# Optimization experiments

Hardware: AMD Instinct MI355X
Metric: run time of the kernel (lower is better)

The kernel has to match this reference:

```python
import jax, jax.numpy as jnp
import numpy as np

B, T, TM = 4, 1024, 1500
D_MODEL, D_FFN, H, D_HEAD, D_MEM = 1024, 4096, 16, 64, 1024
EPS = 1e-5


def layernorm(x, g):
    m = jnp.mean(x, axis=-1, keepdims=True)
    xc = x - m
    v = jnp.mean(xc * xc, axis=-1, keepdims=True)
    return xc * jax.lax.rsqrt(v + EPS) * g


def setup_inputs() -> dict:
    key = jax.random.key(0)
    ks = jax.random.split(key, 12)
    s = lambda fan_in: 1.0 / np.sqrt(fan_in)
    return {
        "x": jax.random.normal(ks[0], (B, T, D_MODEL), jnp.float32),
        "encoder_output": jax.random.normal(ks[1], (B, TM, D_MEM), jnp.float32),
        "encoder_mask": jax.random.randint(ks[2], (B, TM), 0, 2).astype(bool),
        "w_qkv": jax.random.normal(ks[3], (D_MODEL, 3 * H * D_HEAD), jnp.float32) * s(D_MODEL),
        "w_o_sa": jax.random.normal(ks[4], (H * D_HEAD, D_MODEL), jnp.float32) * s(H * D_HEAD),
        "w_q": jax.random.normal(ks[5], (D_MODEL, H * D_HEAD), jnp.float32) * s(D_MODEL),
        "w_kv": jax.random.normal(ks[6], (D_MEM, 2 * H * D_HEAD), jnp.float32) * s(D_MEM),
        "w_o_xa": jax.random.normal(ks[7], (H * D_HEAD, D_MODEL), jnp.float32) * s(H * D_HEAD),
        "w_ff1": jax.random.normal(ks[8], (D_MODEL, D_FFN), jnp.float32) * s(D_MODEL),
        "w_ff2": jax.random.normal(ks[9], (D_FFN, D_MODEL), jnp.float32) * s(D_FFN),
        "g_sa": jnp.ones((D_MODEL,), jnp.float32),
        "g_xaq": jnp.ones((D_MODEL,), jnp.float32),
        "g_xam": jnp.ones((D_MEM,), jnp.float32),
        "g_ff": jnp.ones((D_MODEL,), jnp.float32),
    }


def reference(x, encoder_output, encoder_mask, w_qkv, w_o_sa, w_q, w_kv, w_o_xa,
              w_ff1, w_ff2, g_sa, g_xaq, g_xam, g_ff):
    b, t, _ = x.shape
    scale = D_HEAD ** -0.5

    # ---- causal self-attention ----
    residual = x
    xn = layernorm(x, g_sa)
    qkv = (xn @ w_qkv).reshape(b, t, 3, H, D_HEAD)
    q, k, v = qkv[:, :, 0], qkv[:, :, 1], qkv[:, :, 2]  # (B,T,H,D)
    scores = jnp.einsum('bqhd,bkhd->bhqk', q, k) * scale
    causal = jnp.tril(jnp.ones((t, t), x.dtype))
    scores = scores + (1.0 - causal) * -1e9
    attn = jax.nn.softmax(scores, axis=-1)
    sa = jnp.einsum('bhqk,bkhd->bqhd', attn, v).reshape(b, t, H * D_HEAD)
    x = residual + sa @ w_o_sa

    # ---- cross-attention ----
    residual = x
    qn = layernorm(x, g_xaq)
    mn = layernorm(encoder_output, g_xam)
    tq, tm = t, mn.shape[1]
    qx = (qn @ w_q).reshape(b, tq, H, D_HEAD)
    kvx = (mn @ w_kv).reshape(b, tm, 2, H, D_HEAD)
    kx, vx = kvx[:, :, 0], kvx[:, :, 1]
    xs = jnp.einsum('bqhd,bkhd->bhqk', qx, kx) * scale
    xs = jnp.where(encoder_mask[:, None, None, :], xs, -jnp.inf)
    xattn = jax.nn.softmax(xs, axis=-1)
    xa = jnp.einsum('bhqk,bkhd->bqhd', xattn, vx).reshape(b, tq, H * D_HEAD)
    x = residual + xa @ w_o_xa

    # ---- pointwise FFN (kernel_size=1 conv == linear) ----
    residual = x
    h = layernorm(x, g_ff)
    h = jax.nn.gelu(h @ w_ff1, approximate=True) @ w_ff2
    x = residual + h
    return (x, k, v)
```

## Files before the change

kernel.cpp:

```cpp
#include <hip/hip_runtime.h>
#include <hip/hip_bf16.h>
#include <cstdint>
#include <cstddef>


typedef __attribute__((ext_vector_type(4))) float f32x4;
typedef __attribute__((ext_vector_type(8))) short s8v;
typedef __attribute__((ext_vector_type(2))) unsigned uint2v;

#define DEVI __device__ __forceinline__

DEVI short f2bf(float f) {
  union { float f; unsigned u; } x; x.f = f;
  unsigned r = x.u + 0x7fffu + ((x.u >> 16) & 1u);
  return (short)(r >> 16);
}
DEVI unsigned cvtpk_bf2(float lo, float hi) {
  unsigned r;
  asm("v_cvt_pk_bf16_f32 %0, %1, %2" : "=v"(r) : "v"(lo), "v"(hi));
  return r;
}
DEVI float fexp2(float x) {
  float r;
  asm("v_exp_f32 %0, %1" : "=v"(r) : "v"(x));
  return r;
}
DEVI float bpermf(int srclane, float v) {
  union { float f; int i; } x; x.f = v;
  x.i = __builtin_amdgcn_ds_bpermute(srclane << 2, x.i);
  return x.f;
}
DEVI void gload_lds16(const void* g, void* l) {
  __builtin_amdgcn_global_load_lds((const __attribute__((address_space(1))) void*)g,
                                   (__attribute__((address_space(3))) void*)l,
                                   16, 0, 0);
}

__global__ __launch_bounds__(256) void k_transpose_cvt(
    const float* __restrict__ w, short* __restrict__ wt, int K, int N) {
  __shared__ float tile[32][33];
  int n0 = blockIdx.x * 32, k0 = blockIdx.y * 32;
  int t = threadIdx.x;
  int row = t >> 3, c4 = (t & 7) * 4;
  *(f32x4*)&tile[row][c4] = *(const f32x4*)(w + (size_t)(k0 + row) * N + n0 + c4);
  __syncthreads();
  float v0 = tile[c4 + 0][row], v1 = tile[c4 + 1][row];
  float v2 = tile[c4 + 2][row], v3 = tile[c4 + 3][row];
  uint2v o = {cvtpk_bf2(v0, v1), cvtpk_bf2(v2, v3)};
  *(uint2v*)(wt + (size_t)(n0 + row) * K + k0 + c4) = o;
}

__global__ __launch_bounds__(256) void k_vtrans(
    const short* __restrict__ src, int srs, int coff,
    short* __restrict__ dst, int T, int Tp) {
  __shared__ short tile[32][72];
  int bh = blockIdx.y, b = bh >> 4, h = bh & 15;
  int t0 = blockIdx.x * 32;
  const short* sB = src + (size_t)b * T * srs + coff + h * 64;
  short* dB = dst + (size_t)bh * 64 * Tp;
  int t = threadIdx.x;
  int r = t >> 3, c = (t & 7) * 8;
  int tr = t0 + r; if (tr > T - 1) tr = T - 1;
  *(s8v*)&tile[r][c] = *(const s8v*)(sB + (size_t)tr * srs + c);
  __syncthreads();
  int d = t & 63, ch = t >> 6;
  s8v o;
#pragma unroll
  for (int j = 0; j < 8; j++) o[j] = tile[ch * 8 + j][d];
  *(s8v*)(dB + (size_t)d * Tp + t0 + ch * 8) = o;
}

__global__ void k_maskpack(const int* __restrict__ mask,
                           unsigned long long* __restrict__ out, int Tk, int mw) {
  int b = blockIdx.x, w = threadIdx.x;
  if (w >= mw) return;
  unsigned long long v = 0;
  const int* mb = mask + (size_t)b * Tk;
#pragma unroll 4
  for (int j = 0; j < 64; j++) {
    int k = w * 64 + j;
    if (k < Tk && mb[k]) v |= (1ull << j);
  }
  out[(size_t)b * mw + w] = v;
}

__global__ __launch_bounds__(256) void k_ln(
    const float* __restrict__ x, const float* __restrict__ g,
    short* __restrict__ out) {
  int row = blockIdx.x;
  const float* xr = x + (size_t)row * 1024;
  int t = threadIdx.x, wid = t >> 6, lane = t & 63;
  f32x4 v = ((const f32x4*)xr)[t];
  float s = v[0] + v[1] + v[2] + v[3];
#pragma unroll
  for (int m = 32; m >= 1; m >>= 1) s += __shfl_xor(s, m);
  __shared__ float red[4];
  if (lane == 0) red[wid] = s;
  __syncthreads();
  float mean = (red[0] + red[1] + red[2] + red[3]) * (1.f / 1024.f);
  float q = 0.f;
#pragma unroll
  for (int i = 0; i < 4; i++) { v[i] -= mean; q += v[i] * v[i]; }
#pragma unroll
  for (int m = 32; m >= 1; m >>= 1) q += __shfl_xor(q, m);
  __syncthreads();
  if (lane == 0) red[wid] = q;
  __syncthreads();
  float var = (red[0] + red[1] + red[2] + red[3]) * (1.f / 1024.f);
  float rs = rsqrtf(var + 1e-5f);
  f32x4 gv = ((const f32x4*)g)[t];
  unsigned w0 = cvtpk_bf2(v[0] * rs * gv[0], v[1] * rs * gv[1]);
  unsigned w1 = cvtpk_bf2(v[2] * rs * gv[2], v[3] * rs * gv[3]);
  uint2v w = {w0, w1};
  *(uint2v*)(out + (size_t)row * 1024 + t * 4) = w;
}

template <bool RES, bool GELU_, bool F32OUT, bool BF16OUT, bool KV>
__global__ __launch_bounds__(256) void k_gemm3(
    const short* __restrict__ A, const short* __restrict__ Bt,
    float* __restrict__ Cf, short* __restrict__ Cb,
    const float* __restrict__ res, float* __restrict__ okv,
    int M, int N, int K, int lda, int ldb) {
  __shared__ short As[128 * 64];
  __shared__ short Bs[128 * 64];
  int z = blockIdx.z;
  A += (size_t)z * K;
  Bt += (size_t)z * K;
  if (F32OUT && !RES) Cf += (size_t)z * (size_t)M * N;

  int bx, by;
  {
    int gx = gridDim.x, gy = gridDim.y;
    int nxy = gx * gy, chunk = nxy >> 3;
    int orig = blockIdx.y * gx + blockIdx.x;
    int gid = (orig & 7) * chunk + (orig >> 3);
    int full = gy << 3, nfull = gx >> 3, lim = nfull * full;
    if (gid < lim) {
      int band = gid / full, r = gid - band * full;
      bx = (band << 3) + (r & 7);
      by = r >> 3;
    } else {
      int r = gid - lim, w = gx - (nfull << 3);
      bx = (nfull << 3) + r % w;
      by = r / w;
    }
  }
  int am = bx * 128, bn = by * 128;

  int t = threadIdx.x, wid = t >> 6, lane = t & 63;
  int la = lane & 15, lb = lane >> 4;
  int wr = wid >> 1, wc = wid & 1;

  const short* gp[8];
  int dof[8];
#pragma unroll
  for (int l = 0; l < 8; l++) {
    int cl = (l & 3) * 256 + t;
    int row = cl >> 3, g = cl & 7;
    int col = (g ^ (row & 7)) << 3;
    if (l < 4) {
      int ar = am + row; if (ar > M - 1) ar = M - 1;
      gp[l] = A + (size_t)ar * lda + col;
    } else {
      gp[l] = Bt + (size_t)(bn + row) * ldb + col;
    }
    dof[l] = ((l & 3) * 256 + wid * 64) * 8;
  }

  int aOff[4], bOff[4];
#pragma unroll
  for (int m = 0; m < 4; m++) {
    int r = wr * 64 + m * 16 + la;
    aOff[m] = r * 64 + ((lb ^ (r & 7)) << 3);
  }
#pragma unroll
  for (int n = 0; n < 4; n++) {
    int r = wc * 64 + n * 16 + la;
    bOff[n] = r * 64 + ((lb ^ (r & 7)) << 3);
  }

  f32x4 acc[4][4];
#pragma unroll
  for (int m = 0; m < 4; m++)
#pragma unroll
    for (int n = 0; n < 4; n++) acc[m][n] = (f32x4){0.f, 0.f, 0.f, 0.f};

  int nk = K >> 6;
  for (int ks = 0; ks < nk; ++ks) {
#pragma unroll
    for (int l = 0; l < 4; l++) { gload_lds16(gp[l], As + dof[l]); gp[l] += 64; }
#pragma unroll
    for (int l = 4; l < 8; l++) { gload_lds16(gp[l], Bs + dof[l]); gp[l] += 64; }
    __syncthreads();
#pragma unroll
    for (int kk = 0; kk < 2; kk++) {
      s8v af[4], bfg[4];
#pragma unroll
      for (int m = 0; m < 4; m++)
        af[m] = *(const s8v*)(As + (aOff[m] ^ (kk << 5)));
#pragma unroll
      for (int n = 0; n < 4; n++)
        bfg[n] = *(const s8v*)(Bs + (bOff[n] ^ (kk << 5)));
#pragma unroll
      for (int m = 0; m < 4; m++)
#pragma unroll
        for (int n = 0; n < 4; n++)
          acc[m][n] = __builtin_amdgcn_mfma_f32_16x16x32_bf16(af[m], bfg[n], acc[m][n], 0, 0, 0);
    }
    __syncthreads();
  }

#pragma unroll
  for (int m = 0; m < 4; m++) {
    int rb = am + wr * 64 + m * 16 + lb * 4;
#pragma unroll
    for (int n = 0; n < 4; n++) {
      int col = bn + wc * 64 + n * 16 + la;
#pragma unroll
      for (int j = 0; j < 4; j++) {
        int r = rb + j;
        if (r < M) {
          float v = acc[m][n][j];
          if (RES) v += res[(size_t)r * N + col];
          if (GELU_) {
            float u = v;
            float y = 0.7978845608f * u * (1.f + 0.044715f * u * u);
            float e = fexp2(fminf(y * 2.88539008f, 80.f));
            float th = (e - 1.f) * __builtin_amdgcn_rcpf(e + 1.f);
            v = 0.5f * u * (1.f + th);
          }
          if (F32OUT) Cf[(size_t)r * N + col] = v;
          if (BF16OUT) Cb[(size_t)r * N + col] = f2bf(v);
          if (KV) {
            if (col >= 2048)
              okv[(size_t)4096 * 1024 + (size_t)r * 1024 + (col - 2048)] = v;
            else if (col >= 1024)
              okv[(size_t)r * 1024 + (col - 1024)] = v;
          }
        }
      }
    }
  }
}

__global__ __launch_bounds__(256) void k_red2b(
    const f32x4* __restrict__ p, short* __restrict__ outb, int n) {
  int i = blockIdx.x * 256 + threadIdx.x;
  f32x4 v = p[i] + p[i + (size_t)n];
  uint2v w = {cvtpk_bf2(v[0], v[1]), cvtpk_bf2(v[2], v[3])};
  *(uint2v*)(outb + (size_t)i * 4) = w;
}

__global__ __launch_bounds__(256) void k_red2ln(
    const f32x4* __restrict__ p, const f32x4* __restrict__ res,
    float* __restrict__ xout, short* __restrict__ nout,
    const float* __restrict__ g, int n) {
  int row = blockIdx.x;
  int t = threadIdx.x, wid = t >> 6, lane = t & 63;
  size_t i = (size_t)row * 256 + t;
  f32x4 v = res[i] + (p[i] + p[i + (size_t)n]);
  ((f32x4*)xout)[i] = v;
  float s = v[0] + v[1] + v[2] + v[3];
#pragma unroll
  for (int m = 32; m >= 1; m >>= 1) s += __shfl_xor(s, m);
  __shared__ float red[4];
  if (lane == 0) red[wid] = s;
  __syncthreads();
  float mean = (red[0] + red[1] + red[2] + red[3]) * (1.f / 1024.f);
  float q = 0.f;
#pragma unroll
  for (int k = 0; k < 4; k++) { v[k] -= mean; q += v[k] * v[k]; }
#pragma unroll
  for (int m = 32; m >= 1; m >>= 1) q += __shfl_xor(q, m);
  __syncthreads();
  if (lane == 0) red[wid] = q;
  __syncthreads();
  float var = (red[0] + red[1] + red[2] + red[3]) * (1.f / 1024.f);
  float rs = rsqrtf(var + 1e-5f);
  f32x4 gv = ((const f32x4*)g)[t];
  uint2v w = {cvtpk_bf2(v[0] * rs * gv[0], v[1] * rs * gv[1]),
              cvtpk_bf2(v[2] * rs * gv[2], v[3] * rs * gv[3])};
  *(uint2v*)(nout + (size_t)row * 1024 + t * 4) = w;
}

template <bool CAUSAL>
__global__ __launch_bounds__(512) void k_attn4(
    const short* __restrict__ qbuf, int qrs,
    const short* __restrict__ kbuf, int krs,
    const short* __restrict__ vT, int vts,
    short* __restrict__ obuf, int ors,
    const unsigned long long* __restrict__ mbits, int mwords,
    int Tq, int Tk, float scale) {
  __shared__ short Ks[64 * 64];
  __shared__ short Vs[64 * 64];
  __shared__ short Ps[8 * 1024];
  int lid = blockIdx.y * gridDim.x + blockIdx.x;
  int rest = lid >> 3;
  int bh = (lid & 7) * 8 + (rest & 7);
  int qsel = rest >> 3;
  int b = bh >> 4, h = bh & 15;
  int t = threadIdx.x, wid = t >> 6, lane = t & 63;
  int la = lane & 15, lb = lane >> 4;
  float lscale = scale * 1.44269504f;

  const short* qB = qbuf + (size_t)b * Tq * qrs + h * 64;
  const short* kB = kbuf + (size_t)b * Tk * krs + h * 64;
  const short* vB = vT + (size_t)bh * 64 * vts;
  char* Pw = (char*)(Ps + wid * 1024);

  int sr = t >> 3, scol = (t & 7) * 8;
  int swz = sr * 64 + (scol ^ ((sr & 7) << 3));

  int nsup = CAUSAL ? 2 : 1;
  for (int s = 0; s < nsup; s++) {
    int st = CAUSAL ? (s ? 7 - qsel : qsel) : qsel;
    int q0 = st * 128 + wid * 16;
    int nkt = CAUSAL ? 2 * st + 2 : (Tk + 63) >> 6;
    int lastkt = CAUSAL ? (q0 >> 6) : nkt - 1;

    s8v qf[2];
#pragma unroll
    for (int kk = 0; kk < 2; kk++)
      qf[kk] = *(const s8v*)(qB + (size_t)(q0 + la) * qrs + kk * 32 + lb * 8);

    f32x4 accO[4];
#pragma unroll
    for (int n = 0; n < 4; n++) accO[n] = (f32x4){0.f, 0.f, 0.f, 0.f};
    float m = -1e30f, l = 0.f;

    s8v krg, vrg;
    {
      int tk = sr; if (tk > Tk - 1) tk = Tk - 1;
      krg = *(const s8v*)(kB + (size_t)tk * krs + scol);
      vrg = *(const s8v*)(vB + (size_t)sr * vts + scol);
    }

    for (int kt = 0; kt < nkt; kt++) {
      int kb0 = kt << 6;
      __syncthreads();
      *(s8v*)&Ks[swz] = krg;
      *(s8v*)&Vs[swz] = vrg;
      __syncthreads();
      if (kt + 1 < nkt) {
        int kb = kb0 + 64;
        int tk = kb + sr; if (tk > Tk - 1) tk = Tk - 1;
        krg = *(const s8v*)(kB + (size_t)tk * krs + scol);
        vrg = *(const s8v*)(vB + (size_t)sr * vts + kb + scol);
      }
      if (kt > lastkt) continue;

      bool needMask;
      unsigned long long wm = ~0ull;
      if (CAUSAL) {
        needMask = (kt == lastkt);
      } else {
        wm = mbits[(size_t)b * mwords + kt];
        needMask = (wm != ~0ull);
      }

      float sc[4][4];
      __builtin_amdgcn_s_setprio(1);
#pragma unroll
      for (int n = 0; n < 4; n++) {
        f32x4 a = (f32x4){0.f, 0.f, 0.f, 0.f};
#pragma unroll
        for (int kk = 0; kk < 2; kk++) {
          s8v kf = *(const s8v*)&Ks[(n * 16 + la) * 64 +
                                    ((kk * 32 + lb * 8) ^ ((la & 7) << 3))];
          a = __builtin_amdgcn_mfma_f32_16x16x32_bf16(kf, qf[kk], a, 0, 0, 0);
        }
#pragma unroll
        for (int j = 0; j < 4; j++) {
          float sv = a[j] * lscale;
          if (needMask) {
            int ki = n * 16 + lb * 4 + j;
            bool ok = CAUSAL ? (kb0 + ki <= q0 + la) : (((wm >> ki) & 1ull) != 0);
            sv = ok ? sv : -1e30f;
          }
          sc[n][j] = sv;
        }
      }
      __builtin_amdgcn_s_setprio(0);

      float tm = sc[0][0];
#pragma unroll
      for (int n = 0; n < 4; n++)
#pragma unroll
        for (int j = 0; j < 4; j++) tm = fmaxf(tm, sc[n][j]);
      tm = fmaxf(tm, __shfl_xor(tm, 16));
      tm = fmaxf(tm, __shfl_xor(tm, 32));
      tm = fmaxf(tm, -1e4f);

      bool skip = __all(tm - m <= 10.f);
      float alpha = 1.f;
      if (!skip) {
        float mn_ = fmaxf(m, tm);
        alpha = fexp2(m - mn_);
        m = mn_;
      }

      unsigned W[4][2];
      float ps = 0.f;
#pragma unroll
      for (int n = 0; n < 4; n++) {
        float p0 = fexp2(sc[n][0] - m), p1 = fexp2(sc[n][1] - m);
        float p2 = fexp2(sc[n][2] - m), p3 = fexp2(sc[n][3] - m);
        ps += (p0 + p1) + (p2 + p3);
        W[n][0] = cvtpk_bf2(p0, p1);
        W[n][1] = cvtpk_bf2(p2, p3);
      }
      ps += __shfl_xor(ps, 16);
      ps += __shfl_xor(ps, 32);
      l = l * alpha + ps;

      if (!skip) {
#pragma unroll
        for (int j = 0; j < 4; j++) {
          float aj = bpermf(lb * 20 + j, alpha);
#pragma unroll
          for (int n = 0; n < 4; n++) accO[n][j] *= aj;
        }
      }

#pragma unroll
      for (int n = 0; n < 4; n++) {
        uint2v w2 = {W[n][0], W[n][1]};
        *(uint2v*)(Pw + ((la * 128 + n * 32 + lb * 8) ^ ((la & 7) << 4))) = w2;
      }
      __builtin_amdgcn_s_setprio(1);
#pragma unroll
      for (int kk = 0; kk < 2; kk++) {
        s8v pa = *(const s8v*)(Pw + ((la * 128 + kk * 64 + lb * 16) ^ ((la & 7) << 4)));
#pragma unroll
        for (int n = 0; n < 4; n++) {
          s8v vf = *(const s8v*)&Vs[(n * 16 + la) * 64 +
                                    ((kk * 32 + lb * 8) ^ ((la & 7) << 3))];
          accO[n] = __builtin_amdgcn_mfma_f32_16x16x32_bf16(pa, vf, accO[n], 0, 0, 0);
        }
      }
      __builtin_amdgcn_s_setprio(0);
    }

#pragma unroll
    for (int j = 0; j < 4; j++) {
      float lj = bpermf(lb * 20 + j, l);
      float inv = 1.f / lj;
      int r = q0 + lb * 4 + j;
#pragma unroll
      for (int n = 0; n < 4; n++)
        obuf[(size_t)(b * Tq + r) * ors + h * 64 + n * 16 + la] = f2bf(accO[n][j] * inv);
    }
  }
}

extern "C" void kernel_launch(void* const* d_in, const int* in_sizes, int n_in,
                              void* d_out, int out_size, void* d_ws, size_t ws_size,
                              hipStream_t stream) {
  (void)in_sizes; (void)n_in; (void)out_size; (void)ws_size;
  const float* x      = (const float*)d_in[0];
  const float* enc    = (const float*)d_in[1];
  const int*   mask   = (const int*)d_in[2];
  const float* w_qkv  = (const float*)d_in[3];
  const float* w_o_sa = (const float*)d_in[4];
  const float* w_q    = (const float*)d_in[5];
  const float* w_kv   = (const float*)d_in[6];
  const float* w_o_xa = (const float*)d_in[7];
  const float* w_ff1  = (const float*)d_in[8];
  const float* w_ff2  = (const float*)d_in[9];
  const float* g_sa   = (const float*)d_in[10];
  const float* g_xaq  = (const float*)d_in[11];
  const float* g_xam  = (const float*)d_in[12];
  const float* g_ff   = (const float*)d_in[13];

  float* out_x = (float*)d_out;
  float* out_k = out_x + (size_t)4096 * 1024;

  char* ws = (char*)d_ws;
  size_t off = 0;
  auto alloc = [&](size_t bytes) -> void* {
    void* p = ws + off;
    off += (bytes + 255) & ~(size_t)255;
    return p;
  };
  short* wqkv_t = (short*)alloc((size_t)3072 * 1024 * 2);
  short* wosa_t = (short*)alloc((size_t)1024 * 1024 * 2);
  short* wq_t   = (short*)alloc((size_t)1024 * 1024 * 2);
  short* wkv_t  = (short*)alloc((size_t)2048 * 1024 * 2);
  short* woxa_t = (short*)alloc((size_t)1024 * 1024 * 2);
  short* wff1_t = (short*)alloc((size_t)4096 * 1024 * 2);
  short* wff2_t = (short*)alloc((size_t)1024 * 4096 * 2);
  short* xn     = (short*)alloc((size_t)4096 * 1024 * 2);
  short* qkv_b  = (short*)alloc((size_t)4096 * 3072 * 2);
  short* sa_b   = (short*)alloc((size_t)4096 * 1024 * 2);
  float* x1     = (float*)alloc((size_t)4096 * 1024 * 4);
  short* qn     = (short*)alloc((size_t)4096 * 1024 * 2);
  short* mn     = (short*)alloc((size_t)6000 * 1024 * 2);
  short* qx_b   = (short*)alloc((size_t)4096 * 1024 * 2);
  short* kvx_b  = (short*)alloc((size_t)6000 * 2048 * 2);
  short* xa_b   = (short*)alloc((size_t)4096 * 1024 * 2);
  float* x2     = (float*)alloc((size_t)4096 * 1024 * 4);
  short* hn     = (short*)alloc((size_t)4096 * 1024 * 2);
  short* h1     = (short*)alloc((size_t)4096 * 4096 * 2);
  unsigned long long* mbits = (unsigned long long*)alloc(4 * 24 * 8);

  short* vTsa = xn;
  short* vTxa = h1;
  float* partH = (float*)h1;
  const int NRED = 1048576;

  k_transpose_cvt<<<dim3(96, 32), 256, 0, stream>>>(w_qkv, wqkv_t, 1024, 3072);
  k_transpose_cvt<<<dim3(32, 32), 256, 0, stream>>>(w_o_sa, wosa_t, 1024, 1024);
  k_transpose_cvt<<<dim3(32, 32), 256, 0, stream>>>(w_q, wq_t, 1024, 1024);
  k_transpose_cvt<<<dim3(64, 32), 256, 0, stream>>>(w_kv, wkv_t, 1024, 2048);
  k_transpose_cvt<<<dim3(32, 32), 256, 0, stream>>>(w_o_xa, woxa_t, 1024, 1024);
  k_transpose_cvt<<<dim3(128, 32), 256, 0, stream>>>(w_ff1, wff1_t, 1024, 4096);
  k_transpose_cvt<<<dim3(32, 128), 256, 0, stream>>>(w_ff2, wff2_t, 4096, 1024);
  k_maskpack<<<4, 64, 0, stream>>>(mask, mbits, 1500, 24);

  k_ln<<<4096, 256, 0, stream>>>(x, g_sa, xn);
  k_gemm3<false, false, false, true, true><<<dim3(32, 24), 256, 0, stream>>>(
      xn, wqkv_t, nullptr, qkv_b, nullptr, out_k, 4096, 3072, 1024, 1024, 1024);
  k_vtrans<<<dim3(32, 64), 256, 0, stream>>>(qkv_b, 3072, 2048, vTsa, 1024, 1024);
  k_attn4<true><<<dim3(4, 64), 512, 0, stream>>>(
      qkv_b, 3072, qkv_b + 1024, 3072, vTsa, 1024,
      sa_b, 1024, nullptr, 0, 1024, 1024, 0.125f);
  k_gemm3<false, false, true, false, false><<<dim3(32, 8, 2), 256, 0, stream>>>(
      sa_b, wosa_t, partH, nullptr, nullptr, nullptr, 4096, 1024, 512, 1024, 1024);
  k_red2ln<<<4096, 256, 0, stream>>>(
      (const f32x4*)partH, (const f32x4*)x, x1, qn, g_xaq, NRED);

  k_ln<<<6000, 256, 0, stream>>>(enc, g_xam, mn);
  k_gemm3<false, false, true, false, false><<<dim3(32, 8, 2), 256, 0, stream>>>(
      qn, wq_t, partH, nullptr, nullptr, nullptr, 4096, 1024, 512, 1024, 1024);
  k_red2b<<<4096, 256, 0, stream>>>((const f32x4*)partH, qx_b, NRED);
  k_gemm3<false, false, false, true, false><<<dim3(47, 16), 256, 0, stream>>>(
      mn, wkv_t, nullptr, kvx_b, nullptr, nullptr, 6000, 2048, 1024, 1024, 1024);
  k_vtrans<<<dim3(48, 64), 256, 0, stream>>>(kvx_b, 2048, 1024, vTxa, 1500, 1536);
  k_attn4<false><<<dim3(8, 64), 512, 0, stream>>>(
      qx_b, 1024, kvx_b, 2048, vTxa, 1536,
      xa_b, 1024, mbits, 24, 1024, 1500, 0.125f);
  k_gemm3<false, false, true, false, false><<<dim3(32, 8, 2), 256, 0, stream>>>(
      xa_b, woxa_t, partH, nullptr, nullptr, nullptr, 4096, 1024, 512, 1024, 1024);
  k_red2ln<<<4096, 256, 0, stream>>>(
      (const f32x4*)partH, (const f32x4*)x1, x2, hn, g_ff, NRED);

  k_gemm3<false, true, false, true, false><<<dim3(32, 32), 256, 0, stream>>>(
      hn, wff1_t, nullptr, h1, nullptr, nullptr, 4096, 4096, 1024, 1024, 1024);
  k_gemm3<true, false, true, false, false><<<dim3(32, 8), 256, 0, stream>>>(
      h1, wff2_t, out_x, nullptr, x2, nullptr, 4096, 1024, 4096, 4096, 4096);
}
```

Baseline: 465.8 us.

## Merge prep launches, batch layernorms, and split-K the FFN2 GEMM

Folds the seven weight transpose/convert launches and the mask packing into one k_prep kernel, and runs the decoder and encoder layernorms in a single k_ln2 launch. The FFN down-projection GEMM, which had only 256 tiles over K=4096, becomes a 4-way split-K writing fp32 partials into the reused qkv buffer. A new k_red4 kernel then sums the partials with the residual. This trades launch overhead and low occupancy for an extra 64MB of partial-sum traffic and one more reduction pass.

```diff
diff --git a/kernel.cpp b/kernel.cpp
--- a/kernel.cpp
+++ b/kernel.cpp
@@ -36,10 +36,41 @@
                                    16, 0, 0);
 }
 
-__global__ __launch_bounds__(256) void k_transpose_cvt(
-    const float* __restrict__ w, short* __restrict__ wt, int K, int N) {
+__global__ __launch_bounds__(256) void k_prep(
+    const float* __restrict__ wqkv, const float* __restrict__ wosa,
+    const float* __restrict__ wq,   const float* __restrict__ wkv,
+    const float* __restrict__ woxa, const float* __restrict__ wff1,
+    const float* __restrict__ wff2,
+    short* __restrict__ wqkv_t, short* __restrict__ wosa_t,
+    short* __restrict__ wq_t,   short* __restrict__ wkv_t,
+    short* __restrict__ woxa_t, short* __restrict__ wff1_t,
+    short* __restrict__ wff2_t,
+    const int* __restrict__ mask, unsigned long long* __restrict__ mbits) {
+  int id = blockIdx.x;
+  const float* w; short* wt; int K, N, tx, r;
+  if (id < 3072)       { w = wqkv; wt = wqkv_t; K = 1024; N = 3072; tx = 96;  r = id; }
+  else if (id < 4096)  { w = wosa; wt = wosa_t; K = 1024; N = 1024; tx = 32;  r = id - 3072; }
+  else if (id < 5120)  { w = wq;   wt = wq_t;   K = 1024; N = 1024; tx = 32;  r = id - 4096; }
+  else if (id < 7168)  { w = wkv;  wt = wkv_t;  K = 1024; N = 2048; tx = 64;  r = id - 5120; }
+  else if (id < 8192)  { w = woxa; wt = woxa_t; K = 1024; N = 1024; tx = 32;  r = id - 7168; }
+  else if (id < 12288) { w = wff1; wt = wff1_t; K = 1024; N = 4096; tx = 128; r = id - 8192; }
+  else if (id < 16384) { w = wff2; wt = wff2_t; K = 4096; N = 1024; tx = 32;  r = id - 12288; }
+  else {
+    int t = threadIdx.x;
+    if (t < 96) {
+      int b = t / 24, wd = t % 24;
+      unsigned long long v = 0;
+      const int* mb = mask + (size_t)b * 1500;
+      for (int j = 0; j < 64; j++) {
+        int k = wd * 64 + j;
+        if (k < 1500 && mb[k]) v |= (1ull << j);
+      }
+      mbits[b * 24 + wd] = v;
+    }
+    return;
+  }
   __shared__ float tile[32][33];
-  int n0 = blockIdx.x * 32, k0 = blockIdx.y * 32;
+  int n0 = (r % tx) * 32, k0 = (r / tx) * 32;
   int t = threadIdx.x;
   int row = t >> 3, c4 = (t & 7) * 4;
   *(f32x4*)&tile[row][c4] = *(const f32x4*)(w + (size_t)(k0 + row) * N + n0 + c4);
@@ -70,25 +101,16 @@
   *(s8v*)(dB + (size_t)d * Tp + t0 + ch * 8) = o;
 }
 
-__global__ void k_maskpack(const int* __restrict__ mask,
-                           unsigned long long* __restrict__ out, int Tk, int mw) {
-  int b = blockIdx.x, w = threadIdx.x;
-  if (w >= mw) return;
-  unsigned long long v = 0;
-  const int* mb = mask + (size_t)b * Tk;
-#pragma unroll 4
-  for (int j = 0; j < 64; j++) {
-    int k = w * 64 + j;
-    if (k < Tk && mb[k]) v |= (1ull << j);
-  }
-  out[(size_t)b * mw + w] = v;
-}
-
-__global__ __launch_bounds__(256) void k_ln(
-    const float* __restrict__ x, const float* __restrict__ g,
-    short* __restrict__ out) {
-  int row = blockIdx.x;
-  const float* xr = x + (size_t)row * 1024;
+__global__ __launch_bounds__(256) void k_ln2(
+    const float* __restrict__ x, const float* __restrict__ gx,
+    short* __restrict__ ox,
+    const float* __restrict__ e, const float* __restrict__ ge,
+    short* __restrict__ oe) {
+  int id = blockIdx.x;
+  const float* src; const float* g; short* dst; int row;
+  if (id < 4096) { src = x; g = gx; dst = ox; row = id; }
+  else           { src = e; g = ge; dst = oe; row = id - 4096; }
+  const float* xr = src + (size_t)row * 1024;
   int t = threadIdx.x, wid = t >> 6, lane = t & 63;
   f32x4 v = ((const f32x4*)xr)[t];
   float s = v[0] + v[1] + v[2] + v[3];
@@ -109,10 +131,9 @@
   float var = (red[0] + red[1] + red[2] + red[3]) * (1.f / 1024.f);
   float rs = rsqrtf(var + 1e-5f);
   f32x4 gv = ((const f32x4*)g)[t];
-  unsigned w0 = cvtpk_bf2(v[0] * rs * gv[0], v[1] * rs * gv[1]);
-  unsigned w1 = cvtpk_bf2(v[2] * rs * gv[2], v[3] * rs * gv[3]);
-  uint2v w = {w0, w1};
-  *(uint2v*)(out + (size_t)row * 1024 + t * 4) = w;
+  uint2v w = {cvtpk_bf2(v[0] * rs * gv[0], v[1] * rs * gv[1]),
+              cvtpk_bf2(v[2] * rs * gv[2], v[3] * rs * gv[3])};
+  *(uint2v*)(dst + (size_t)row * 1024 + t * 4) = w;
 }
 
 template <bool RES, bool GELU_, bool F32OUT, bool BF16OUT, bool KV>
@@ -249,6 +270,15 @@
   f32x4 v = p[i] + p[i + (size_t)n];
   uint2v w = {cvtpk_bf2(v[0], v[1]), cvtpk_bf2(v[2], v[3])};
   *(uint2v*)(outb + (size_t)i * 4) = w;
+}
+
+__global__ __launch_bounds__(256) void k_red4(
+    const f32x4* __restrict__ p, const f32x4* __restrict__ res,
+    float* __restrict__ outf, int n) {
+  int i = blockIdx.x * 256 + threadIdx.x;
+  f32x4 v = res[i] + ((p[i] + p[i + (size_t)n]) +
+                      (p[i + 2 * (size_t)n] + p[i + 3 * (size_t)n]));
+  ((f32x4*)outf)[i] = v;
 }
 
 __global__ __launch_bounds__(256) void k_red2ln(
@@ -506,18 +536,14 @@
   short* vTsa = xn;
   short* vTxa = h1;
   float* partH = (float*)h1;
+  float* partQ = (float*)qkv_b;
   const int NRED = 1048576;
 
-  k_transpose_cvt<<<dim3(96, 32), 256, 0, stream>>>(w_qkv, wqkv_t, 1024, 3072);
-  k_transpose_cvt<<<dim3(32, 32), 256, 0, stream>>>(w_o_sa, wosa_t, 1024, 1024);
-  k_transpose_cvt<<<dim3(32, 32), 256, 0, stream>>>(w_q, wq_t, 1024, 1024);
-  k_transpose_cvt<<<dim3(64, 32), 256, 0, stream>>>(w_kv, wkv_t, 1024, 2048);
-  k_transpose_cvt<<<dim3(32, 32), 256, 0, stream>>>(w_o_xa, woxa_t, 1024, 1024);
-  k_transpose_cvt<<<dim3(128, 32), 256, 0, stream>>>(w_ff1, wff1_t, 1024, 4096);
-  k_transpose_cvt<<<dim3(32, 128), 256, 0, stream>>>(w_ff2, wff2_t, 4096, 1024);
-  k_maskpack<<<4, 64, 0, stream>>>(mask, mbits, 1500, 24);
-
-  k_ln<<<4096, 256, 0, stream>>>(x, g_sa, xn);
+  k_prep<<<16385, 256, 0, stream>>>(
+      w_qkv, w_o_sa, w_q, w_kv, w_o_xa, w_ff1, w_ff2,
+      wqkv_t, wosa_t, wq_t, wkv_t, woxa_t, wff1_t, wff2_t, mask, mbits);
+  k_ln2<<<10096, 256, 0, stream>>>(x, g_sa, xn, enc, g_xam, mn);
+
   k_gemm3<false, false, false, true, true><<<dim3(32, 24), 256, 0, stream>>>(
       xn, wqkv_t, nullptr, qkv_b, nullptr, out_k, 4096, 3072, 1024, 1024, 1024);
   k_vtrans<<<dim3(32, 64), 256, 0, stream>>>(qkv_b, 3072, 2048, vTsa, 1024, 1024);
@@ -529,7 +555,6 @@
   k_red2ln<<<4096, 256, 0, stream>>>(
       (const f32x4*)partH, (const f32x4*)x, x1, qn, g_xaq, NRED);
 
-  k_ln<<<6000, 256, 0, stream>>>(enc, g_xam, mn);
   k_gemm3<false, false, true, false, false><<<dim3(32, 8, 2), 256, 0, stream>>>(
       qn, wq_t, partH, nullptr, nullptr, nullptr, 4096, 1024, 512, 1024, 1024);
   k_red2b<<<4096, 256, 0, stream>>>((const f32x4*)partH, qx_b, NRED);
@@ -546,6 +571,8 @@
 
   k_gemm3<false, true, false, true, false><<<dim3(32, 32), 256, 0, stream>>>(
       hn, wff1_t, nullptr, h1, nullptr, nullptr, 4096, 4096, 1024, 1024, 1024);
-  k_gemm3<true, false, true, false, false><<<dim3(32, 8), 256, 0, stream>>>(
-      h1, wff2_t, out_x, nullptr, x2, nullptr, 4096, 1024, 4096, 4096, 4096);
-}
+  k_gemm3<false, false, true, false, false><<<dim3(32, 8, 4), 256, 0, stream>>>(
+      h1, wff2_t, partQ, nullptr, nullptr, nullptr, 4096, 1024, 1024, 4096, 4096);
+  k_red4<<<4096, 256, 0, stream>>>(
+      (const f32x4*)partQ, (const f32x4*)x2, out_x, NRED);
+}
```

New measurement: 417.6 us. 1.12x faster.
